# Performance work log

Measured on AMD Instinct MI355X. Metric: run time of the kernel, lower is better.

The kernel has to match this reference:

```python
import jax, jax.numpy as jnp
import numpy as np

N = 64000   # nodes
E = 256000  # edges
G = 2000    # graphs
D = 300     # emb_dim
H = 4       # heads
C = D // H  # head dim = 75
L = 5       # layers
ED = 32     # edge_emb_dim
FD = 256    # feat_dim


def _ln(x, g, b):
    m = x.mean(-1, keepdims=True)
    v = jnp.mean((x - m) ** 2, axis=-1, keepdims=True)
    return (x - m) * jax.lax.rsqrt(v + 1e-5) * g + b


def setup_inputs() -> dict:
    key = jax.random.key(0)
    ks = iter(jax.random.split(key, 48))
    def nrm(shape, s=0.02):
        return jax.random.normal(next(ks), shape, jnp.float32) * s
    inp = {}
    inp["x"] = jax.random.randint(next(ks), (N, 2), 0, 3)
    inp["edge_index"] = jax.random.randint(next(ks), (2, E), 0, N)
    inp["edge_attr"] = jax.random.randint(next(ks), (E, 2), 0, 3)
    inp["batch"] = jnp.sort(jax.random.randint(next(ks), (N,), 0, G))
    inp.update(dict(
        x_emb1=nrm((119, D)), x_emb2=nrm((3, D)),
        e_emb_t=nrm((5, ED)), e_emb_d=nrm((3, ED)),
        edge_proj_w=nrm((ED, ED)), edge_proj_b=nrm((ED,)),
        q_w=nrm((L, D, D)), q_b=nrm((L, D)),
        k_w=nrm((L, D, D)), k_b=nrm((L, D)),
        v_w=nrm((L, D, D)), v_b=nrm((L, D)),
        e_w=nrm((L, ED, D)),
        skip_w=nrm((L, D, D)), skip_b=nrm((L, D)),
        ln1_g=jnp.ones((L, D), jnp.float32), ln1_b=jnp.zeros((L, D), jnp.float32),
        ln2_g=jnp.ones((L, D), jnp.float32), ln2_b=jnp.zeros((L, D), jnp.float32),
        ffn_w1=nrm((L, D, 4 * D)), ffn_b1=nrm((L, 4 * D)),
        ffn_w2=nrm((L, 4 * D, D)), ffn_b2=nrm((L, D)),
        feat_w=nrm((D, FD)), feat_b=nrm((FD,)),
        out_w1=nrm((FD, FD)), out_b1=nrm((FD,)),
        out_w2=nrm((FD, FD // 2)), out_b2=nrm((FD // 2,)),
    ))
    return inp


def reference(x, edge_index, edge_attr, batch, x_emb1, x_emb2, e_emb_t, e_emb_d,
              edge_proj_w, edge_proj_b, q_w, q_b, k_w, k_b, v_w, v_b, e_w,
              skip_w, skip_b, ln1_g, ln1_b, ln2_g, ln2_b,
              ffn_w1, ffn_b1, ffn_w2, ffn_b2, feat_w, feat_b,
              out_w1, out_b1, out_w2, out_b2):
    # node / edge embeddings
    h = x_emb1[x[:, 0]] + x_emb2[x[:, 1]]                               # [N, D]
    ef = (e_emb_t[edge_attr[:, 0]] + e_emb_d[edge_attr[:, 1]]) @ edge_proj_w + edge_proj_b  # [E, ED]
    src, dst = edge_index[0], edge_index[1]
    scale = 1.0 / np.sqrt(C).astype(np.float32)
    for l in range(L):  # loop over fixed layer count
        q = (h @ q_w[l] + q_b[l]).reshape(N, H, C)
        k = (h @ k_w[l] + k_b[l]).reshape(N, H, C)
        v = (h @ v_w[l] + v_b[l]).reshape(N, H, C)
        e = (ef @ e_w[l]).reshape(E, H, C)
        kj = k[src] + e                                                 # [E, H, C]
        alpha = jnp.einsum('ehc,ehc->eh', q[dst], kj) * scale           # [E, H]
        amax = jax.lax.stop_gradient(jax.ops.segment_max(alpha, dst, num_segments=N))
        ea = jnp.exp(alpha - amax[dst])
        den = jax.ops.segment_sum(ea, dst, num_segments=N)
        attn = ea / den[dst]                                            # segment softmax over in-edges of dst
        msg = attn[:, :, None] * (v[src] + e)
        agg = jax.ops.segment_sum(msg, dst, num_segments=N).reshape(N, D)
        conv = agg + h @ skip_w[l] + skip_b[l]                          # TransformerConv with root skip
        h = _ln(h + conv, ln1_g[l], ln1_b[l])
        f = jax.nn.relu(h @ ffn_w1[l] + ffn_b1[l]) @ ffn_w2[l] + ffn_b2[l]
        h = _ln(h + f, ln2_g[l], ln2_b[l])
    cnt = jax.ops.segment_sum(jnp.ones((N,), jnp.float32), batch, num_segments=G)
    g = jax.ops.segment_sum(h, batch, num_segments=G) / jnp.clip(cnt, 1.0)[:, None]
    g = g @ feat_w + feat_b                                             # [G, FD]
    out = jax.nn.relu(g @ out_w1 + out_b1) @ out_w2 + out_b2            # [G, FD//2]
    return (g, out)
```

## Files before the change

### kernel.cpp

```cpp
#include <hip/hip_runtime.h>
#include <hip/hip_bf16.h>
#include <math.h>

typedef __hip_bfloat16 bf16;
typedef unsigned short ushort_t;
typedef unsigned int uint_t;

using bf16x8 = __attribute__((ext_vector_type(8))) __bf16;
using f32x4  = __attribute__((ext_vector_type(4))) float;

constexpr int kN  = 64000;
constexpr int kE  = 256000;
constexpr int kG  = 2000;
constexpr int kD  = 300;
constexpr int kH  = 4;
constexpr int kC  = 75;
constexpr int kL  = 5;
constexpr int kED = 32;
constexpr int kFD = 256;
constexpr int kT  = 15;
constexpr int kDp = 320;
constexpr int kKp2 = 1216;
constexpr int kQV = 1280;
constexpr int kQVn = 1264;
constexpr int kOffK = 300, kOffV = 600, kOffS = 900, kOffQE = 1200;
constexpr int kNpW1 = 1280, kNpW2 = 384;
constexpr int kFDp = 304;

static inline int cdiv(int a, int b) { return (a + b - 1) / b; }

__device__ __forceinline__ ushort_t f2bf(float f) {
    uint_t u = __float_as_uint(f);
    uint_t r = u + 0x7FFFu + ((u >> 16) & 1u);
    return (ushort_t)(r >> 16);
}
__device__ __forceinline__ float bu2f(ushort_t u) {
    return __uint_as_float(((uint_t)u) << 16);
}

__device__ __forceinline__ void gld_lds16(const ushort_t* g, ushort_t* l)
{
    __builtin_amdgcn_global_load_lds(
        (const __attribute__((address_space(1))) void*)g,
        (__attribute__((address_space(3))) void*)(uint_t)(unsigned long long)l,
        16, 0, 0);
}

__global__ void detect_kernel(const uint_t* __restrict__ w, int* __restrict__ flag)
{
    if (threadIdx.x == 0 && blockIdx.x == 0)
        *flag = (w[0] == 0x3F803F80u) ? 1 : 0;
}

__global__ void cvt_kernel(const void* __restrict__ in, float* __restrict__ out,
                           long long n, const int* __restrict__ flag)
{
    long long i = (long long)blockIdx.x * 256 + threadIdx.x;
    if (i >= n) return;
    if (*flag) out[i] = bu2f(((const ushort_t*)in)[i]);
    else       out[i] = ((const float*)in)[i];
}

__global__ void out_write_kernel(const float* __restrict__ in, void* __restrict__ out,
                                 long long n, long long eoff, const int* __restrict__ flag)
{
    long long i = (long long)blockIdx.x * 256 + threadIdx.x;
    if (i >= n) return;
    if (*flag) ((bf16*)out)[eoff + i] = __float2bfloat16(in[i]);
    else       ((float*)out)[eoff + i] = in[i];
}

__global__ void wt_kernel(const void* __restrict__ W, long long elemOff,
                          ushort_t* __restrict__ WT,
                          int K, int N, int ldk, const int* __restrict__ flag)
{
    int i = blockIdx.x * 256 + threadIdx.x;
    if (i >= K * N) return;
    int k = i / N, n = i % N;
    ushort_t val;
    if (*flag) val = ((const ushort_t*)W)[elemOff + i];
    else       val = f2bf(((const float*)W)[elemOff + i]);
    WT[(size_t)n * ldk + k] = val;
}

__global__ void biasqkvs_kernel(const float* __restrict__ qb, const float* __restrict__ kb,
                                const float* __restrict__ vb, const float* __restrict__ sb,
                                float* __restrict__ out)
{
    int i = blockIdx.x * 256 + threadIdx.x;
    if (i >= kL * kQV) return;
    int l = i / kQV, c = i % kQV;
    float v = 0.f;
    if (c < kOffK)          v = qb[l * kD + c];
    else if (c < kOffV)     v = kb[l * kD + c - kOffK];
    else if (c < kOffS)     v = vb[l * kD + c - kOffV];
    else if (c < kOffQE)    v = sb[l * kD + c - kOffS];
    out[i] = v;
}

constexpr int gBM = 128, gBN = 128, gBK = 32;
constexpr int kEpiLd = 136;

__global__ __launch_bounds__(256) void mgemm_kernel(
    const ushort_t* __restrict__ A, int lda,
    const ushort_t* __restrict__ BT, int ldb,
    const float* __restrict__ bias,
    ushort_t* __restrict__ outB, int ldob,
    int M, int N, int K, int relu)
{
    __shared__ ushort_t smem[gBM * kEpiLd];
    ushort_t* As = smem;
    ushort_t* Bs = smem + 8192;

    const int tid  = threadIdx.x;

    const int nxg = gridDim.x;
    int bid;
    {
        int nb = nxg * gridDim.y;
        int orig = blockIdx.y * nxg + blockIdx.x;
        int q8 = nb >> 3, r8 = nb & 7;
        int xcd = orig & 7, lid = orig >> 3;
        bid = (xcd < r8 ? xcd * (q8 + 1) : r8 * (q8 + 1) + (xcd - r8) * q8) + lid;
    }
    const int bm = (bid / nxg) * gBM;
    const int bn = (bid % nxg) * gBN;

    const int wave = tid >> 6, lane = tid & 63;
    const int wr = wave >> 1, wc = wave & 1;
    const int lq = lane & 15, qd = lane >> 4;
    const int qs = (qd ^ ((lq >> 1) & 3)) * 8;

    f32x4 acc[4][4];
#pragma unroll
    for (int i = 0; i < 4; i++)
#pragma unroll
        for (int j = 0; j < 4; j++) acc[i][j] = (f32x4){0.f, 0.f, 0.f, 0.f};

    {
#pragma unroll
        for (int p = 0; p < 2; p++) {
            int u = tid + p * 256;
            gld_lds16(A + (size_t)(bm + (u >> 2)) * lda + ((u ^ (u >> 3)) & 3) * 8, As + u * 8);
        }
#pragma unroll
        for (int p = 0; p < 2; p++) {
            int u = tid + p * 256;
            gld_lds16(BT + (size_t)(bn + (u >> 2)) * ldb + ((u ^ (u >> 3)) & 3) * 8, Bs + u * 8);
        }
    }
    __syncthreads();

    const int nk = K / gBK;
    for (int kt = 0; kt < nk; kt++) {
        const int cb = (kt & 1) * 4096;

        bf16x8 af[4], bfg[4];
#pragma unroll
        for (int i = 0; i < 4; i++)
            af[i] = *reinterpret_cast<const bf16x8*>(&As[cb + (wr * 64 + i * 16 + lq) * gBK + qs]);
#pragma unroll
        for (int j = 0; j < 4; j++)
            bfg[j] = *reinterpret_cast<const bf16x8*>(&Bs[cb + (wc * 64 + j * 16 + lq) * gBK + qs]);

        if (kt + 1 < nk) {
            const int k0 = (kt + 1) * gBK;
            const int nb2 = cb ^ 4096;
#pragma unroll
            for (int p = 0; p < 2; p++) {
                int u = tid + p * 256;
                gld_lds16(A + (size_t)(bm + (u >> 2)) * lda + k0 + ((u ^ (u >> 3)) & 3) * 8,
                          As + nb2 + u * 8);
            }
#pragma unroll
            for (int p = 0; p < 2; p++) {
                int u = tid + p * 256;
                gld_lds16(BT + (size_t)(bn + (u >> 2)) * ldb + k0 + ((u ^ (u >> 3)) & 3) * 8,
                          Bs + nb2 + u * 8);
            }
        }

#pragma unroll
        for (int i = 0; i < 4; i++)
#pragma unroll
            for (int j = 0; j < 4; j++)
                acc[i][j] = __builtin_amdgcn_mfma_f32_16x16x32_bf16(af[i], bfg[j], acc[i][j], 0, 0, 0);

        __syncthreads();
    }

#pragma unroll
    for (int i = 0; i < 4; i++) {
#pragma unroll
        for (int j = 0; j < 4; j++) {
            int lcol = wc * 64 + j * 16 + lq;
            int gcol = bn + lcol;
            float bv = (bias && gcol < N) ? bias[gcol] : 0.f;
#pragma unroll
            for (int r2 = 0; r2 < 4; r2++) {
                int lrow = wr * 64 + i * 16 + qd * 4 + r2;
                float v = acc[i][j][r2] + bv;
                if (relu) v = fmaxf(v, 0.f);
                smem[lrow * kEpiLd + lcol] = f2bf(v);
            }
        }
    }
    __syncthreads();
#pragma unroll
    for (int s = 0; s < 8; s++) {
        int seg  = tid + s * 256;
        int lrow = seg >> 4;
        int loff = (seg & 15) * 8;
        int gcol = bn + loff;
        if (gcol + 8 <= ldob) {
            bf16x8 pv = *reinterpret_cast<const bf16x8*>(&smem[lrow * kEpiLd + loff]);
            *reinterpret_cast<bf16x8*>(&outB[(size_t)(bm + lrow) * ldob + gcol]) = pv;
        }
    }
}

__global__ __launch_bounds__(256) void gemm_kernel(
    const float* __restrict__ A, const float* __restrict__ W,
    const float* __restrict__ bias, float* __restrict__ C,
    int M, int N, int K, int relu)
{
    constexpr int BM = 64, BN = 64, BK = 16;
    __shared__ float As[BK][BM + 1];
    __shared__ float Bs[BK][BN + 1];
    const int bm = blockIdx.y * BM;
    const int bn = blockIdx.x * BN;
    const int tid = threadIdx.x;
    const int tr = tid / 16;
    const int tc = tid % 16;
    float acc[4][4] = {};
    for (int k0 = 0; k0 < K; k0 += BK) {
        for (int t = tid; t < BM * BK; t += 256) {
            int r = t / BK, c = t % BK;
            int gr = bm + r, gc = k0 + c;
            As[c][r] = (gr < M && gc < K) ? A[(size_t)gr * K + gc] : 0.f;
        }
        for (int t = tid; t < BK * BN; t += 256) {
            int r = t / BN, c = t % BN;
            int gr = k0 + r, gc = bn + c;
            Bs[r][c] = (gr < K && gc < N) ? W[(size_t)gr * N + gc] : 0.f;
        }
        __syncthreads();
#pragma unroll
        for (int k = 0; k < BK; k++) {
            float a[4], b[4];
#pragma unroll
            for (int i = 0; i < 4; i++) a[i] = As[k][tr * 4 + i];
#pragma unroll
            for (int j = 0; j < 4; j++) b[j] = Bs[k][tc * 4 + j];
#pragma unroll
            for (int i = 0; i < 4; i++)
#pragma unroll
                for (int j = 0; j < 4; j++) acc[i][j] += a[i] * b[j];
        }
        __syncthreads();
    }
#pragma unroll
    for (int i = 0; i < 4; i++) {
        int gr = bm + tr * 4 + i;
        if (gr >= M) continue;
#pragma unroll
        for (int j = 0; j < 4; j++) {
            int gc = bn + tc * 4 + j;
            if (gc >= N) continue;
            float v = acc[i][j];
            if (bias) v += bias[gc];
            if (relu) v = fmaxf(v, 0.f);
            C[(size_t)gr * N + gc] = v;
        }
    }
}

__global__ void node_embed_kernel(const int* __restrict__ x,
                                  const float* __restrict__ emb1,
                                  const float* __restrict__ emb2,
                                  ushort_t* __restrict__ hb)
{
    long long i = (long long)blockIdx.x * blockDim.x + threadIdx.x;
    if (i >= (long long)kN * kD) return;
    int n = (int)(i / kD), d = (int)(i % kD);
    float v = emb1[(size_t)x[n * 2] * kD + d] + emb2[(size_t)x[n * 2 + 1] * kD + d];
    hb[(size_t)n * kDp + d] = f2bf(v);
}

__global__ void eftab_kernel(const float* __restrict__ emb_t, const float* __restrict__ emb_d,
                             const float* __restrict__ pw, const float* __restrict__ pb,
                             float* __restrict__ eftab)
{
    int tid = threadIdx.x;
    if (tid >= kT * kED) return;
    int t = tid / kED, j = tid % kED;
    int a0 = t / 3, a1 = t % 3;
    float acc = pb[j];
#pragma unroll
    for (int k = 0; k < kED; k++) {
        float s = emb_t[a0 * kED + k] + emb_d[a1 * kED + k];
        acc += s * pw[k * kED + j];
    }
    eftab[tid] = acc;
}

__global__ __launch_bounds__(256) void etab_kernel(const float* __restrict__ eftab,
                                                   const float* __restrict__ ew,
                                                   float* __restrict__ etab)
{
    __shared__ float se[kT * kED];
    for (int i = threadIdx.x; i < kT * kED; i += 256) se[i] = eftab[i];
    __syncthreads();
    for (int o = threadIdx.x; o < kT * kD; o += 256) {
        int t = o / kD, d = o % kD;
        float acc = 0.f;
#pragma unroll
        for (int k = 0; k < kED; k++) acc += se[t * kED + k] * ew[k * kD + d];
        etab[o] = acc;
    }
}

__global__ void etabT2_kernel(const float* __restrict__ etab, ushort_t* __restrict__ out)
{
    int i = blockIdx.x * 256 + threadIdx.x;
    if (i >= 64 * kDp) return;
    int j = i / kDp, k = i % kDp;
    ushort_t v = 0;
    if (j < kT * kH && k < kD) {
        int t = j >> 2, hh = j & 3;
        if (k >= hh * kC && k < hh * kC + kC) v = f2bf(etab[t * kD + k]);
    }
    out[i] = v;
}

__global__ void izero_kernel(int* __restrict__ p, int n)
{
    int i = blockIdx.x * 256 + threadIdx.x;
    if (i < n) p[i] = 0;
}

__global__ void deg_kernel(const int* __restrict__ dst, int* __restrict__ deg)
{
    int e = blockIdx.x * 256 + threadIdx.x;
    if (e >= kE) return;
    atomicAdd(&deg[dst[e]], 1);
}

__global__ __launch_bounds__(256) void scan1_kernel(const int* __restrict__ deg, int* __restrict__ bsum)
{
    __shared__ int s[256];
    int i = blockIdx.x * 256 + threadIdx.x;
    s[threadIdx.x] = (i < kN) ? deg[i] : 0;
    __syncthreads();
    for (int off = 128; off > 0; off >>= 1) {
        if (threadIdx.x < off) s[threadIdx.x] += s[threadIdx.x + off];
        __syncthreads();
    }
    if (threadIdx.x == 0) bsum[blockIdx.x] = s[0];
}

__global__ __launch_bounds__(256) void scan2_kernel(const int* __restrict__ bsum, int* __restrict__ boff,
                                                    int nb, int* __restrict__ row_ptr)
{
    __shared__ int s[256];
    int tid = threadIdx.x;
    int v = (tid < nb) ? bsum[tid] : 0;
    s[tid] = v;
    __syncthreads();
    for (int off = 1; off < 256; off <<= 1) {
        int t = (tid >= off) ? s[tid - off] : 0;
        __syncthreads();
        s[tid] += t;
        __syncthreads();
    }
    if (tid < nb) boff[tid] = s[tid] - v;
    if (tid == 255) row_ptr[kN] = s[255];
}

__global__ __launch_bounds__(256) void scan3_kernel(const int* __restrict__ deg, const int* __restrict__ boff,
                                                    int* __restrict__ row_ptr)
{
    __shared__ int s[256];
    int tid = threadIdx.x;
    int i = blockIdx.x * 256 + tid;
    int v = (i < kN) ? deg[i] : 0;
    s[tid] = v;
    __syncthreads();
    for (int off = 1; off < 256; off <<= 1) {
        int t = (tid >= off) ? s[tid - off] : 0;
        __syncthreads();
        s[tid] += t;
        __syncthreads();
    }
    if (i < kN) row_ptr[i] = boff[blockIdx.x] + s[tid] - v;
}

__global__ void poscopy_kernel(const int* __restrict__ row_ptr, int* __restrict__ pos)
{
    int i = blockIdx.x * 256 + threadIdx.x;
    if (i < kN) pos[i] = row_ptr[i];
}

__global__ void fill_kernel(const int* __restrict__ src, const int* __restrict__ dst,
                            const int* __restrict__ edge_attr,
                            int* __restrict__ pos, int* __restrict__ cpack)
{
    int e = blockIdx.x * 256 + threadIdx.x;
    if (e >= kE) return;
    int d = dst[e];
    int slot = atomicAdd(&pos[d], 1);
    cpack[slot] = (src[e] << 8) | (edge_attr[e * 2] * 3 + edge_attr[e * 2 + 1]);
}

__global__ void gptr_kernel(const int* __restrict__ batch, int* __restrict__ gptr)
{
    int i = blockIdx.x * 256 + threadIdx.x;
    if (i >= kN) return;
    int b1 = batch[i];
    int b0 = (i == 0) ? -1 : batch[i - 1];
    for (int g = b0 + 1; g <= b1; g++) gptr[g] = i;
    if (i == kN - 1)
        for (int g = b1 + 1; g <= kG; g++) gptr[g] = kN;
}

__global__ __launch_bounds__(256) void gsln_kernel(
    const int* __restrict__ row_ptr, const int* __restrict__ cpack,
    const ushort_t* __restrict__ qkvs,
    const float* __restrict__ etab,
    const float* __restrict__ g, const float* __restrict__ b,
    ushort_t* __restrict__ hb)
{
    __shared__ float sE[kT * kD];
    for (int i = threadIdx.x; i < kT * kD; i += 256) sE[i] = etab[i];
    __syncthreads();
    const int wslot = threadIdx.x >> 6, lane = threadIdx.x & 63;
    const int hh = lane >> 4, sub = lane & 15;
    const float scale = 0.11547005383792516f;

    int idxj[5];
    bool vj[5];
#pragma unroll
    for (int j = 0; j < 5; j++) {
        int o = sub + 16 * j;
        vj[j] = (o < kC);
        idxj[j] = hh * kC + (vj[j] ? o : 0);
    }

    for (int it = 0; it < 4; it++) {
        int n = blockIdx.x * 4 + wslot + it * 16000;
        int beg = row_ptr[n], end = row_ptr[n + 1];
        const ushort_t* qrow = qkvs + (size_t)n * kQV;

        float qv[5];
#pragma unroll
        for (int j = 0; j < 5; j++)
            qv[j] = vj[j] ? bu2f(qrow[idxj[j]]) : 0.f;

        float acc[5] = {0.f, 0.f, 0.f, 0.f, 0.f};
        float den = 0.f;
        for (int i = beg; i < end; i++) {
            int pk = cpack[i];
            int s = pk >> 8, t = pk & 255;
            const ushort_t* srow = qkvs + (size_t)s * kQV;
            float hp = 0.f;
#pragma unroll
            for (int j = 0; j < 5; j++)
                if (vj[j]) hp += qv[j] * bu2f(srow[kOffK + idxj[j]]);
            hp += __shfl_xor(hp, 1, 64);
            hp += __shfl_xor(hp, 2, 64);
            hp += __shfl_xor(hp, 4, 64);
            hp += __shfl_xor(hp, 8, 64);
            float a = (hp + bu2f(qrow[kOffQE + t * kH + hh])) * scale;
            a = fminf(fmaxf(a, -60.f), 60.f);
            float eh = expf(a);
            den += eh;
            const float* ep = sE + t * kD;
#pragma unroll
            for (int j = 0; j < 5; j++)
                if (vj[j]) acc[j] += eh * (bu2f(srow[kOffV + idxj[j]]) + ep[idxj[j]]);
        }

        const float inv_den = (den > 0.f) ? 1.f / den : 0.f;
        const ushort_t* skipp = qrow + kOffS;
        float vals[5], sum = 0.f;
#pragma unroll
        for (int j = 0; j < 5; j++) {
            float tV = 0.f;
            if (vj[j])
                tV = bu2f(hb[(size_t)n * kDp + idxj[j]]) + acc[j] * inv_den + bu2f(skipp[idxj[j]]);
            vals[j] = tV;
            sum += tV;
        }
        for (int off = 1; off < 64; off <<= 1) sum += __shfl_xor(sum, off, 64);
        float mean = sum / kD;
        float var = 0.f;
#pragma unroll
        for (int j = 0; j < 5; j++) {
            if (vj[j]) { float dv = vals[j] - mean; var += dv * dv; }
        }
        for (int off = 1; off < 64; off <<= 1) var += __shfl_xor(var, off, 64);
        float rstd = rsqrtf(var / kD + 1e-5f);
#pragma unroll
        for (int j = 0; j < 5; j++) {
            if (vj[j])
                hb[(size_t)n * kDp + idxj[j]] =
                    f2bf((vals[j] - mean) * rstd * g[idxj[j]] + b[idxj[j]]);
        }
    }
}

__global__ __launch_bounds__(256) void ln2_kernel(
    ushort_t* hb, const ushort_t* __restrict__ f, int ldf,
    const float* __restrict__ g, const float* __restrict__ b)
{
    int row  = (blockIdx.x * blockDim.x + threadIdx.x) >> 6;
    int lane = threadIdx.x & 63;
    if (row >= kN) return;
    size_t baseH = (size_t)row * kDp;
    size_t baseF = (size_t)row * ldf;
    float vals[5];
    float sum = 0.f;
#pragma unroll
    for (int i = 0; i < 5; i++) {
        int idx = lane + i * 64;
        float t = 0.f;
        if (idx < kD) t = bu2f(hb[baseH + idx]) + bu2f(f[baseF + idx]);
        vals[i] = t;
        sum += t;
    }
    for (int off = 1; off < 64; off <<= 1) sum += __shfl_xor(sum, off, 64);
    float mean = sum / kD;
    float var = 0.f;
#pragma unroll
    for (int i = 0; i < 5; i++) {
        int idx = lane + i * 64;
        if (idx < kD) { float dv = vals[i] - mean; var += dv * dv; }
    }
    for (int off = 1; off < 64; off <<= 1) var += __shfl_xor(var, off, 64);
    float rstd = rsqrtf(var / kD + 1e-5f);
#pragma unroll
    for (int i = 0; i < 5; i++) {
        int idx = lane + i * 64;
        if (idx < kD)
            hb[baseH + idx] = f2bf((vals[i] - mean) * rstd * g[idx] + b[idx]);
    }
}

__global__ void zero_kernel(float* __restrict__ p, long long n)
{
    long long i = (long long)blockIdx.x * blockDim.x + threadIdx.x;
    if (i < n) p[i] = 0.f;
}

__global__ __launch_bounds__(256) void pool2_kernel(const ushort_t* __restrict__ hb,
                                                    const int* __restrict__ gptr,
                                                    float* __restrict__ pooled)
{
    int g = blockIdx.x;
    int beg = gptr[g], end = gptr[g + 1];
    float inv = (end > beg) ? 1.f / (float)(end - beg) : 0.f;
    for (int d = threadIdx.x; d < kD; d += 256) {
        float acc = 0.f;
        for (int n = beg; n < end; n++)
            acc += bu2f(hb[(size_t)n * kDp + d]);
        pooled[(size_t)g * kD + d] = acc * inv;
    }
}

extern "C" void kernel_launch(void* const* d_in, const int* in_sizes, int n_in,
                              void* d_out, int out_size, void* d_ws, size_t ws_size,
                              hipStream_t stream)
{
    const int* x          = (const int*)d_in[0];
    const int* edge_index = (const int*)d_in[1];
    const int* edge_attr  = (const int*)d_in[2];
    const int* batch      = (const int*)d_in[3];
    const int* src = edge_index;
    const int* dst = edge_index + kE;

    float* ws = (float*)d_ws;
    size_t off = 0;
    int* flag = (int*)(ws + off); off += 16;
    const bool big[33] = {false,false,false,false,false,false,false,false,false,false,
                          true, false, true, false, true, false, false, true, false, false,
                          false,false,false, true, false, true, false,false,false,false,
                          false,false,false};
    float* canon[33] = {};
    for (int i = 4; i < 33; i++) {
        if (big[i]) continue;
        canon[i] = ws + off; off += (size_t)in_sizes[i];
    }
    off = (off + 3) & ~(size_t)3;
    int* deg     = (int*)(ws + off); off += (size_t)kN;
    int* row_ptr = (int*)(ws + off); off += (size_t)kN + 4;
    int* pos     = (int*)(ws + off); off += (size_t)kN;
    int* cpack   = (int*)(ws + off); off += (size_t)kE;
    int* bsum    = (int*)(ws + off); off += 256;
    int* boff    = (int*)(ws + off); off += 256;
    int* gptr    = (int*)(ws + off); off += (size_t)kG + 4;
    float* eftab = ws + off; off += (size_t)kT * kED;
    float* etab5 = ws + off; off += (size_t)kL * kT * kD;
    float* bqv5  = ws + off; off += (size_t)kL * kQV;
    off = (off + 3) & ~(size_t)3;
    ushort_t* hb   = (ushort_t*)(ws + off); off += (size_t)kN * kDp / 2;
    ushort_t* QV   = (ushort_t*)(ws + off); off += (size_t)kN * kQV / 2;
    ushort_t* fbuf = (ushort_t*)(ws + off); off += (size_t)kN * kFDp / 2;
    ushort_t* warena = (ushort_t*)(ws + off);
    ushort_t* wqv5 = warena;
    ushort_t* wt15 = wqv5 + (size_t)kL * kQV * kDp;
    ushort_t* wt25 = wt15 + (size_t)kL * kNpW1 * kDp;
    size_t warena_ushorts = (size_t)kL * (kQV + kNpW1) * kDp + (size_t)kL * kNpW2 * kKp2;
    off += warena_ushorts / 2 + 4;
    float* pooled = (float*)QV;
    float* gbuf   = pooled + (size_t)kG * kD;
    float* t1     = gbuf + (size_t)kG * kFD;
    float* o2     = t1 + (size_t)kG * kFD;

    detect_kernel<<<1, 64, 0, stream>>>((const uint_t*)d_in[19], flag);
    for (int i = 4; i < 33; i++) {
        if (big[i]) continue;
        long long n = in_sizes[i];
        cvt_kernel<<<cdiv((int)n, 256), 256, 0, stream>>>(d_in[i], canon[i], n, flag);
    }

    const long long ND = (long long)kN * kD;

    auto mgemm = [&](const ushort_t* A, int lda, const ushort_t* BT, int ldb,
                     const float* bias, ushort_t* outB, int ldob,
                     int M, int N, int K, int relu) {
        dim3 grid(cdiv(N, 128), M / 128);
        mgemm_kernel<<<grid, 256, 0, stream>>>(A, lda, BT, ldb, bias, outB, ldob, M, N, K, relu);
    };
    auto gemm = [&](const float* A, const float* W, const float* bias, float* C,
                    int M, int N, int K, int relu) {
        dim3 grid(cdiv(N, 64), cdiv(M, 64));
        gemm_kernel<<<grid, 256, 0, stream>>>(A, W, bias, C, M, N, K, relu);
    };

    node_embed_kernel<<<cdiv((int)ND, 256), 256, 0, stream>>>(x, canon[4], canon[5], hb);
    eftab_kernel<<<1, 512, 0, stream>>>(canon[6], canon[7], canon[8], canon[9], eftab);

    const int nb = cdiv(kN, 256);
    izero_kernel<<<cdiv(kN, 256), 256, 0, stream>>>(deg, kN);
    deg_kernel<<<cdiv(kE, 256), 256, 0, stream>>>(dst, deg);
    scan1_kernel<<<nb, 256, 0, stream>>>(deg, bsum);
    scan2_kernel<<<1, 256, 0, stream>>>(bsum, boff, nb, row_ptr);
    scan3_kernel<<<nb, 256, 0, stream>>>(deg, boff, row_ptr);
    poscopy_kernel<<<cdiv(kN, 256), 256, 0, stream>>>(row_ptr, pos);
    fill_kernel<<<cdiv(kE, 256), 256, 0, stream>>>(src, dst, edge_attr, pos, cpack);
    gptr_kernel<<<cdiv(kN, 256), 256, 0, stream>>>(batch, gptr);

    zero_kernel<<<cdiv((int)(warena_ushorts / 2), 256) + 1, 256, 0, stream>>>(
        (float*)warena, (long long)(warena_ushorts / 2));
    for (int l = 0; l < kL; l++) {
        ushort_t* wqv = wqv5 + (size_t)l * kQV * kDp;
        ushort_t* w1  = wt15 + (size_t)l * kNpW1 * kDp;
        ushort_t* w2  = wt25 + (size_t)l * kNpW2 * kKp2;
        float* etab   = etab5 + (size_t)l * kT * kD;
        wt_kernel<<<cdiv(kD * kD, 256), 256, 0, stream>>>(d_in[10], (long long)l * kD * kD, wqv, kD, kD, kDp, flag);
        wt_kernel<<<cdiv(kD * kD, 256), 256, 0, stream>>>(d_in[12], (long long)l * kD * kD, wqv + (size_t)kOffK * kDp, kD, kD, kDp, flag);
        wt_kernel<<<cdiv(kD * kD, 256), 256, 0, stream>>>(d_in[14], (long long)l * kD * kD, wqv + (size_t)kOffV * kDp, kD, kD, kDp, flag);
        wt_kernel<<<cdiv(kD * kD, 256), 256, 0, stream>>>(d_in[17], (long long)l * kD * kD, wqv + (size_t)kOffS * kDp, kD, kD, kDp, flag);
        wt_kernel<<<cdiv(kD * 1200, 256), 256, 0, stream>>>(d_in[23], (long long)l * kD * 1200, w1, kD, 1200, kDp, flag);
        wt_kernel<<<cdiv(1200 * kD, 256), 256, 0, stream>>>(d_in[25], (long long)l * 1200 * kD, w2, 1200, kD, kKp2, flag);
        etab_kernel<<<1, 256, 0, stream>>>(eftab, canon[16] + (size_t)l * kED * kD, etab);
        etabT2_kernel<<<cdiv(64 * kDp, 256), 256, 0, stream>>>(etab, wqv + (size_t)kOffQE * kDp);
    }
    biasqkvs_kernel<<<cdiv(kL * kQV, 256), 256, 0, stream>>>(
        canon[11], canon[13], canon[15], canon[18], bqv5);

    for (int l = 0; l < kL; l++) {
        const ushort_t* wqv = wqv5 + (size_t)l * kQV * kDp;
        const ushort_t* w1  = wt15 + (size_t)l * kNpW1 * kDp;
        const ushort_t* w2  = wt25 + (size_t)l * kNpW2 * kKp2;
        const float* etab = etab5 + (size_t)l * kT * kD;

        mgemm(hb, kDp, wqv, kDp, bqv5 + (size_t)l * kQV, QV, kQV, kN, kQVn, kDp, 0);

        gsln_kernel<<<4000, 256, 0, stream>>>(row_ptr, cpack, QV, etab,
            canon[19] + (size_t)l * kD, canon[20] + (size_t)l * kD, hb);

        ushort_t* mid = QV;
        mgemm(hb, kDp, w1, kDp, canon[24] + (size_t)l * 1200, mid, kKp2,
              kN, 1200, kDp, 1);
        mgemm(mid, kKp2, w2, kKp2, canon[26] + (size_t)l * kD, fbuf, kFDp,
              kN, kD, kKp2, 0);

        ln2_kernel<<<kN / 4, 256, 0, stream>>>(hb, fbuf, kFDp,
            canon[21] + (size_t)l * kD, canon[22] + (size_t)l * kD);
    }

    pool2_kernel<<<kG, 256, 0, stream>>>(hb, gptr, pooled);

    gemm(pooled, canon[27], canon[28], gbuf, kG, kFD, kD, 0);
    gemm(gbuf, canon[29], canon[30], t1, kG, kFD, kFD, 1);
    gemm(t1, canon[31], canon[32], o2, kG, kFD / 2, kFD, 0);

    out_write_kernel<<<cdiv(kG * kFD, 256), 256, 0, stream>>>(
        gbuf, d_out, (long long)kG * kFD, 0, flag);
    out_write_kernel<<<cdiv(kG * kFD / 2, 256), 256, 0, stream>>>(
        o2, d_out, (long long)kG * (kFD / 2), (long long)kG * kFD, flag);
}
```

Measured before the change: 2.564 ms.

## Fuse FFN up and down projections into one kernel keeping intermediate in LDS

Replaces the two FFN GEMMs with a single fused kernel. Each 1024-thread block handles 128 rows. It computes relu(h@W1+b1) in 128-column chunks, stages each chunk in shared memory as bf16, and accumulates it straight into the W2 projection. This removes the write and re-read of the N x 1216 intermediate through global memory. In exchange, A and W operands are read directly from global memory without LDS tiling, and only 500 blocks launch, which may limit occupancy and MFMA efficiency.

```diff
diff --git a/kernel.cpp b/kernel.cpp
--- a/kernel.cpp
+++ b/kernel.cpp
@@ -20,11 +20,11 @@
 constexpr int kFD = 256;
 constexpr int kT  = 15;
 constexpr int kDp = 320;
-constexpr int kKp2 = 1216;
 constexpr int kQV = 1280;
 constexpr int kQVn = 1264;
 constexpr int kOffK = 300, kOffV = 600, kOffS = 900, kOffQE = 1200;
 constexpr int kNpW1 = 1280, kNpW2 = 384;
+constexpr int kW2ld = 1280;
 constexpr int kFDp = 304;
 
 static inline int cdiv(int a, int b) { return (a + b - 1) / b; }
@@ -216,6 +216,131 @@
             bf16x8 pv = *reinterpret_cast<const bf16x8*>(&smem[lrow * kEpiLd + loff]);
             *reinterpret_cast<bf16x8*>(&outB[(size_t)(bm + lrow) * ldob + gcol]) = pv;
         }
+    }
+}
+
+__global__ __launch_bounds__(1024) void ffn_kernel(
+    const ushort_t* __restrict__ A,
+    const ushort_t* __restrict__ W1T,
+    const ushort_t* __restrict__ W2T,
+    const float* __restrict__ b1,
+    const float* __restrict__ b2,
+    ushort_t* __restrict__ outF)
+{
+    __shared__ ushort_t sm[64 * 328];
+
+    int bid;
+    {
+        int nb = gridDim.x, orig = blockIdx.x;
+        int q8 = nb >> 3, r8 = nb & 7;
+        int xcd = orig & 7, lid = orig >> 3;
+        bid = (xcd < r8 ? xcd * (q8 + 1) : r8 * (q8 + 1) + (xcd - r8) * q8) + lid;
+    }
+    const int bm = bid * 128;
+
+    const int tid  = threadIdx.x;
+    const int wave = tid >> 6, lane = tid & 63;
+    const int wr = wave >> 2, wc = wave & 3;
+    const int lq = lane & 15, qd = lane >> 4, qk = qd * 8;
+
+    f32x4 acc2[2][5];
+#pragma unroll
+    for (int i = 0; i < 2; i++)
+#pragma unroll
+        for (int j = 0; j < 5; j++) acc2[i][j] = (f32x4){0.f, 0.f, 0.f, 0.f};
+
+    const ushort_t* a0 = A + (size_t)(bm + wr * 32 + lq) * kDp;
+    const ushort_t* a1 = A + (size_t)(bm + wr * 32 + 16 + lq) * kDp;
+
+    for (int j = 0; j < 10; j++) {
+        const int jc = j * 128;
+
+        f32x4 macc[2][2];
+#pragma unroll
+        for (int i = 0; i < 2; i++)
+#pragma unroll
+            for (int q = 0; q < 2; q++) macc[i][q] = (f32x4){0.f, 0.f, 0.f, 0.f};
+
+        const ushort_t* w1p0 = W1T + (size_t)(jc + wc * 32 + lq) * kDp;
+        const ushort_t* w1p1 = w1p0 + (size_t)16 * kDp;
+#pragma unroll 2
+        for (int kt = 0; kt < 10; kt++) {
+            const int ko = kt * 32 + qk;
+            bf16x8 af0 = *reinterpret_cast<const bf16x8*>(a0 + ko);
+            bf16x8 af1 = *reinterpret_cast<const bf16x8*>(a1 + ko);
+            bf16x8 bg0 = *reinterpret_cast<const bf16x8*>(w1p0 + ko);
+            bf16x8 bg1 = *reinterpret_cast<const bf16x8*>(w1p1 + ko);
+            macc[0][0] = __builtin_amdgcn_mfma_f32_16x16x32_bf16(af0, bg0, macc[0][0], 0, 0, 0);
+            macc[0][1] = __builtin_amdgcn_mfma_f32_16x16x32_bf16(af0, bg1, macc[0][1], 0, 0, 0);
+            macc[1][0] = __builtin_amdgcn_mfma_f32_16x16x32_bf16(af1, bg0, macc[1][0], 0, 0, 0);
+            macc[1][1] = __builtin_amdgcn_mfma_f32_16x16x32_bf16(af1, bg1, macc[1][1], 0, 0, 0);
+        }
+
+        float bv1[2];
+#pragma unroll
+        for (int q = 0; q < 2; q++) {
+            int c1 = jc + wc * 32 + q * 16 + lq;
+            bv1[q] = (c1 < 1200) ? b1[c1] : 0.f;
+        }
+#pragma unroll
+        for (int i = 0; i < 2; i++)
+#pragma unroll
+            for (int q = 0; q < 2; q++)
+#pragma unroll
+                for (int r2 = 0; r2 < 4; r2++) {
+                    int row = wr * 32 + i * 16 + qd * 4 + r2;
+                    int col = wc * 32 + q * 16 + lq;
+                    sm[row * 136 + col] = f2bf(fmaxf(macc[i][q][r2] + bv1[q], 0.f));
+                }
+        __syncthreads();
+
+#pragma unroll 2
+        for (int kt2 = 0; kt2 < 4; kt2++) {
+            const int ko = kt2 * 32 + qk;
+            bf16x8 mf0 = *reinterpret_cast<const bf16x8*>(&sm[(wr * 32 + lq) * 136 + ko]);
+            bf16x8 mf1 = *reinterpret_cast<const bf16x8*>(&sm[(wr * 32 + 16 + lq) * 136 + ko]);
+#pragma unroll
+            for (int j5 = 0; j5 < 5; j5++) {
+                bf16x8 wg = *reinterpret_cast<const bf16x8*>(
+                    W2T + (size_t)(wc * 80 + j5 * 16 + lq) * kW2ld + jc + ko);
+                acc2[0][j5] = __builtin_amdgcn_mfma_f32_16x16x32_bf16(mf0, wg, acc2[0][j5], 0, 0, 0);
+                acc2[1][j5] = __builtin_amdgcn_mfma_f32_16x16x32_bf16(mf1, wg, acc2[1][j5], 0, 0, 0);
+            }
+        }
+        __syncthreads();
+    }
+
+    float bv2[5];
+#pragma unroll
+    for (int j5 = 0; j5 < 5; j5++) {
+        int col = wc * 80 + j5 * 16 + lq;
+        bv2[j5] = (col < kD) ? b2[col] : 0.f;
+    }
+#pragma unroll
+    for (int h = 0; h < 2; h++) {
+        if ((wr >> 1) == h) {
+#pragma unroll
+            for (int i = 0; i < 2; i++)
+#pragma unroll
+                for (int j5 = 0; j5 < 5; j5++)
+#pragma unroll
+                    for (int r2 = 0; r2 < 4; r2++) {
+                        int row = (wr & 1) * 32 + i * 16 + qd * 4 + r2;
+                        int col = wc * 80 + j5 * 16 + lq;
+                        sm[row * 328 + col] = f2bf(acc2[i][j5][r2] + bv2[j5]);
+                    }
+        }
+        __syncthreads();
+#pragma unroll
+        for (int p = 0; p < 3; p++) {
+            int seg = tid + p * 1024;
+            if (seg < 64 * 38) {
+                int row = seg / 38, c8 = (seg % 38) * 8;
+                bf16x8 pv = *reinterpret_cast<const bf16x8*>(&sm[row * 328 + c8]);
+                *reinterpret_cast<bf16x8*>(&outF[(size_t)(bm + h * 64 + row) * kFDp + c8]) = pv;
+            }
+        }
+        __syncthreads();
     }
 }
 
@@ -609,7 +734,7 @@
     ushort_t* wqv5 = warena;
     ushort_t* wt15 = wqv5 + (size_t)kL * kQV * kDp;
     ushort_t* wt25 = wt15 + (size_t)kL * kNpW1 * kDp;
-    size_t warena_ushorts = (size_t)kL * (kQV + kNpW1) * kDp + (size_t)kL * kNpW2 * kKp2;
+    size_t warena_ushorts = (size_t)kL * (kQV + kNpW1) * kDp + (size_t)kL * kNpW2 * kW2ld;
     off += warena_ushorts / 2 + 4;
     float* pooled = (float*)QV;
     float* gbuf   = pooled + (size_t)kG * kD;
@@ -655,14 +780,14 @@
     for (int l = 0; l < kL; l++) {
         ushort_t* wqv = wqv5 + (size_t)l * kQV * kDp;
         ushort_t* w1  = wt15 + (size_t)l * kNpW1 * kDp;
-        ushort_t* w2  = wt25 + (size_t)l * kNpW2 * kKp2;
+        ushort_t* w2  = wt25 + (size_t)l * kNpW2 * kW2ld;
         float* etab   = etab5 + (size_t)l * kT * kD;
         wt_kernel<<<cdiv(kD * kD, 256), 256, 0, stream>>>(d_in[10], (long long)l * kD * kD, wqv, kD, kD, kDp, flag);
         wt_kernel<<<cdiv(kD * kD, 256), 256, 0, stream>>>(d_in[12], (long long)l * kD * kD, wqv + (size_t)kOffK * kDp, kD, kD, kDp, flag);
         wt_kernel<<<cdiv(kD * kD, 256), 256, 0, stream>>>(d_in[14], (long long)l * kD * kD, wqv + (size_t)kOffV * kDp, kD, kD, kDp, flag);
         wt_kernel<<<cdiv(kD * kD, 256), 256, 0, stream>>>(d_in[17], (long long)l * kD * kD, wqv + (size_t)kOffS * kDp, kD, kD, kDp, flag);
         wt_kernel<<<cdiv(kD * 1200, 256), 256, 0, stream>>>(d_in[23], (long long)l * kD * 1200, w1, kD, 1200, kDp, flag);
-        wt_kernel<<<cdiv(1200 * kD, 256), 256, 0, stream>>>(d_in[25], (long long)l * 1200 * kD, w2, 1200, kD, kKp2, flag);
+        wt_kernel<<<cdiv(1200 * kD, 256), 256, 0, stream>>>(d_in[25], (long long)l * 1200 * kD, w2, 1200, kD, kW2ld, flag);
         etab_kernel<<<1, 256, 0, stream>>>(eftab, canon[16] + (size_t)l * kED * kD, etab);
         etabT2_kernel<<<cdiv(64 * kDp, 256), 256, 0, stream>>>(etab, wqv + (size_t)kOffQE * kDp);
     }
@@ -672,7 +797,7 @@
     for (int l = 0; l < kL; l++) {
         const ushort_t* wqv = wqv5 + (size_t)l * kQV * kDp;
         const ushort_t* w1  = wt15 + (size_t)l * kNpW1 * kDp;
-        const ushort_t* w2  = wt25 + (size_t)l * kNpW2 * kKp2;
+        const ushort_t* w2  = wt25 + (size_t)l * kNpW2 * kW2ld;
         const float* etab = etab5 + (size_t)l * kT * kD;
 
         mgemm(hb, kDp, wqv, kDp, bqv5 + (size_t)l * kQV, QV, kQV, kN, kQVn, kDp, 0);
@@ -680,11 +805,8 @@
         gsln_kernel<<<4000, 256, 0, stream>>>(row_ptr, cpack, QV, etab,
             canon[19] + (size_t)l * kD, canon[20] + (size_t)l * kD, hb);
 
-        ushort_t* mid = QV;
-        mgemm(hb, kDp, w1, kDp, canon[24] + (size_t)l * 1200, mid, kKp2,
-              kN, 1200, kDp, 1);
-        mgemm(mid, kKp2, w2, kKp2, canon[26] + (size_t)l * kD, fbuf, kFDp,
-              kN, kD, kKp2, 0);
+        ffn_kernel<<<500, 1024, 0, stream>>>(hb, w1, w2,
+            canon[24] + (size_t)l * 1200, canon[26] + (size_t)l * kD, fbuf);
 
         ln2_kernel<<<kN / 4, 256, 0, stream>>>(hb, fbuf, kFDp,
             canon[21] + (size_t)l * kD, canon[22] + (size_t)l * kD);
```

After: 4.474 ms. +74.5%, slower.

## Fuse FFN second GEMM with residual LayerNorm and batch edge gather loop

Applied to the files above, without the earlier changes.

Replaces the separate FFN down-projection GEMM plus ln2 kernel with one kernel. It computes a 128-row by 320-column tile with MFMA, then applies bias, the residual add and LayerNorm from shared memory, so the fbuf intermediate no longer makes a round trip through global memory. Separately, the attention gather loop now processes four edges per iteration with batched loads, interleaved shuffles and a fast exp, to expose more memory-level parallelism. The fused kernel uses large shared memory and 20 accumulators per thread, which may limit occupancy, and it adds a zeroing pass over hb.

```diff
diff --git a/kernel.cpp b/kernel.cpp
--- a/kernel.cpp
+++ b/kernel.cpp
@@ -25,7 +25,7 @@
 constexpr int kQVn = 1264;
 constexpr int kOffK = 300, kOffV = 600, kOffS = 900, kOffQE = 1200;
 constexpr int kNpW1 = 1280, kNpW2 = 384;
-constexpr int kFDp = 304;
+constexpr int kW2ld = 1280;
 
 static inline int cdiv(int a, int b) { return (a + b - 1) / b; }
 
@@ -216,6 +216,131 @@
             bf16x8 pv = *reinterpret_cast<const bf16x8*>(&smem[lrow * kEpiLd + loff]);
             *reinterpret_cast<bf16x8*>(&outB[(size_t)(bm + lrow) * ldob + gcol]) = pv;
         }
+    }
+}
+
+__global__ __launch_bounds__(512, 4) void ffn2ln_kernel(
+    const ushort_t* __restrict__ A,
+    const ushort_t* __restrict__ BT,
+    const float* __restrict__ b2,
+    ushort_t* hb,
+    const float* __restrict__ g, const float* __restrict__ b)
+{
+    __shared__ ushort_t smem[28672];
+    ushort_t* As = smem;
+    ushort_t* Bs = smem + 8192;
+
+    int bid;
+    {
+        int nb = gridDim.x, orig = blockIdx.x;
+        int q8 = nb >> 3, r8 = nb & 7;
+        int xcd = orig & 7, lid = orig >> 3;
+        bid = (xcd < r8 ? xcd * (q8 + 1) : r8 * (q8 + 1) + (xcd - r8) * q8) + lid;
+    }
+    const int bm = bid * 128;
+
+    const int tid  = threadIdx.x;
+    const int wave = tid >> 6, lane = tid & 63;
+    const int wr = wave >> 1, wc = wave & 1;
+    const int lq = lane & 15, qd = lane >> 4;
+    const int qs = (qd ^ ((lq >> 1) & 3)) * 8;
+
+    auto stage = [&](int kt, int buf) {
+        const int k0 = kt * 32;
+        {
+            int u = tid;
+            gld_lds16(A + (size_t)(bm + (u >> 2)) * kKp2 + k0 + ((u ^ (u >> 3)) & 3) * 8,
+                      As + buf * 4096 + u * 8);
+        }
+#pragma unroll
+        for (int p = 0; p < 3; p++) {
+            int u = tid + p * 512;
+            if (u < 1280)
+                gld_lds16(BT + (size_t)(u >> 2) * kW2ld + k0 + ((u ^ (u >> 3)) & 3) * 8,
+                          Bs + buf * 10240 + u * 8);
+        }
+    };
+
+    f32x4 acc[2][10];
+#pragma unroll
+    for (int i = 0; i < 2; i++)
+#pragma unroll
+        for (int f = 0; f < 10; f++) acc[i][f] = (f32x4){0.f, 0.f, 0.f, 0.f};
+
+    stage(0, 0);
+    __syncthreads();
+
+    for (int kt = 0; kt < kKp2 / 32; kt++) {
+        const int cur = kt & 1;
+        bf16x8 af0 = *reinterpret_cast<const bf16x8*>(
+            &As[cur * 4096 + (wr * 32 + lq) * 32 + qs]);
+        bf16x8 af1 = *reinterpret_cast<const bf16x8*>(
+            &As[cur * 4096 + (wr * 32 + 16 + lq) * 32 + qs]);
+        if (kt + 1 < kKp2 / 32) stage(kt + 1, cur ^ 1);
+#pragma unroll
+        for (int f = 0; f < 10; f++) {
+            bf16x8 bfg = *reinterpret_cast<const bf16x8*>(
+                &Bs[cur * 10240 + (wc * 160 + f * 16 + lq) * 32 + qs]);
+            acc[0][f] = __builtin_amdgcn_mfma_f32_16x16x32_bf16(af0, bfg, acc[0][f], 0, 0, 0);
+            acc[1][f] = __builtin_amdgcn_mfma_f32_16x16x32_bf16(af1, bfg, acc[1][f], 0, 0, 0);
+        }
+        __syncthreads();
+    }
+
+    float bv[10];
+#pragma unroll
+    for (int f = 0; f < 10; f++) {
+        int col = wc * 160 + f * 16 + lq;
+        bv[f] = (col < kD) ? b2[col] : 0.f;
+    }
+    const int team = tid >> 6;
+#pragma unroll
+    for (int h = 0; h < 2; h++) {
+        if ((wr >> 1) == h) {
+#pragma unroll
+            for (int i = 0; i < 2; i++)
+#pragma unroll
+                for (int f = 0; f < 10; f++)
+#pragma unroll
+                    for (int r2 = 0; r2 < 4; r2++) {
+                        int row = (wr & 1) * 32 + i * 16 + qd * 4 + r2;
+                        int col = wc * 160 + f * 16 + lq;
+                        smem[row * 328 + col] = f2bf(acc[i][f][r2] + bv[f]);
+                    }
+        }
+        __syncthreads();
+        for (int r = 0; r < 8; r++) {
+            int rl = team * 8 + r;
+            int n = bm + h * 64 + rl;
+            size_t baseH = (size_t)n * kDp;
+            float vals[5];
+            float sum = 0.f;
+#pragma unroll
+            for (int i5 = 0; i5 < 5; i5++) {
+                int idx = lane + i5 * 64;
+                float t = 0.f;
+                if (idx < kD) t = bu2f(hb[baseH + idx]) + bu2f(smem[rl * 328 + idx]);
+                vals[i5] = t;
+                sum += t;
+            }
+            for (int off2 = 1; off2 < 64; off2 <<= 1) sum += __shfl_xor(sum, off2, 64);
+            float mean = sum / kD;
+            float var = 0.f;
+#pragma unroll
+            for (int i5 = 0; i5 < 5; i5++) {
+                int idx = lane + i5 * 64;
+                if (idx < kD) { float dv = vals[i5] - mean; var += dv * dv; }
+            }
+            for (int off2 = 1; off2 < 64; off2 <<= 1) var += __shfl_xor(var, off2, 64);
+            float rstd = rsqrtf(var / kD + 1e-5f);
+#pragma unroll
+            for (int i5 = 0; i5 < 5; i5++) {
+                int idx = lane + i5 * 64;
+                if (idx < kD)
+                    hb[baseH + idx] = f2bf((vals[i5] - mean) * rstd * g[idx] + b[idx]);
+            }
+        }
+        __syncthreads();
     }
 }
 
@@ -458,26 +583,58 @@
 
         float acc[5] = {0.f, 0.f, 0.f, 0.f, 0.f};
         float den = 0.f;
-        for (int i = beg; i < end; i++) {
-            int pk = cpack[i];
-            int s = pk >> 8, t = pk & 255;
-            const ushort_t* srow = qkvs + (size_t)s * kQV;
-            float hp = 0.f;
-#pragma unroll
-            for (int j = 0; j < 5; j++)
-                if (vj[j]) hp += qv[j] * bu2f(srow[kOffK + idxj[j]]);
-            hp += __shfl_xor(hp, 1, 64);
-            hp += __shfl_xor(hp, 2, 64);
-            hp += __shfl_xor(hp, 4, 64);
-            hp += __shfl_xor(hp, 8, 64);
-            float a = (hp + bu2f(qrow[kOffQE + t * kH + hh])) * scale;
-            a = fminf(fmaxf(a, -60.f), 60.f);
-            float eh = expf(a);
-            den += eh;
-            const float* ep = sE + t * kD;
-#pragma unroll
-            for (int j = 0; j < 5; j++)
-                if (vj[j]) acc[j] += eh * (bu2f(srow[kOffV + idxj[j]]) + ep[idxj[j]]);
+        for (int i = beg; i < end; i += 4) {
+            int pk[4];
+            float ehm[4];
+#pragma unroll
+            for (int e = 0; e < 4; e++) {
+                bool hv = (i + e < end);
+                pk[e] = cpack[hv ? i + e : i];
+                ehm[e] = hv ? 1.f : 0.f;
+            }
+            const ushort_t* sr[4];
+            int tt[4];
+#pragma unroll
+            for (int e = 0; e < 4; e++) {
+                sr[e] = qkvs + (size_t)(pk[e] >> 8) * kQV;
+                tt[e] = pk[e] & 255;
+            }
+            float kv[4][5];
+#pragma unroll
+            for (int e = 0; e < 4; e++)
+#pragma unroll
+                for (int j = 0; j < 5; j++)
+                    kv[e][j] = vj[j] ? bu2f(sr[e][kOffK + idxj[j]]) : 0.f;
+            float qe[4];
+#pragma unroll
+            for (int e = 0; e < 4; e++)
+                qe[e] = bu2f(qrow[kOffQE + tt[e] * kH + hh]);
+
+            float hp[4] = {0.f, 0.f, 0.f, 0.f};
+#pragma unroll
+            for (int e = 0; e < 4; e++)
+#pragma unroll
+                for (int j = 0; j < 5; j++) hp[e] += qv[j] * kv[e][j];
+#pragma unroll
+            for (int m = 1; m <= 8; m <<= 1) {
+#pragma unroll
+                for (int e = 0; e < 4; e++) hp[e] += __shfl_xor(hp[e], m, 64);
+            }
+            float eh[4];
+#pragma unroll
+            for (int e = 0; e < 4; e++) {
+                float a = fminf(fmaxf((hp[e] + qe[e]) * scale, -60.f), 60.f);
+                eh[e] = __expf(a) * ehm[e];
+                den += eh[e];
+            }
+#pragma unroll
+            for (int e = 0; e < 4; e++) {
+                const float* ep = sE + tt[e] * kD;
+#pragma unroll
+                for (int j = 0; j < 5; j++)
+                    if (vj[j])
+                        acc[j] += eh[e] * (bu2f(sr[e][kOffV + idxj[j]]) + ep[idxj[j]]);
+            }
         }
 
         const float inv_den = (den > 0.f) ? 1.f / den : 0.f;
@@ -506,43 +663,6 @@
                 hb[(size_t)n * kDp + idxj[j]] =
                     f2bf((vals[j] - mean) * rstd * g[idxj[j]] + b[idxj[j]]);
         }
-    }
-}
-
-__global__ __launch_bounds__(256) void ln2_kernel(
-    ushort_t* hb, const ushort_t* __restrict__ f, int ldf,
-    const float* __restrict__ g, const float* __restrict__ b)
-{
-    int row  = (blockIdx.x * blockDim.x + threadIdx.x) >> 6;
-    int lane = threadIdx.x & 63;
-    if (row >= kN) return;
-    size_t baseH = (size_t)row * kDp;
-    size_t baseF = (size_t)row * ldf;
-    float vals[5];
-    float sum = 0.f;
-#pragma unroll
-    for (int i = 0; i < 5; i++) {
-        int idx = lane + i * 64;
-        float t = 0.f;
-        if (idx < kD) t = bu2f(hb[baseH + idx]) + bu2f(f[baseF + idx]);
-        vals[i] = t;
-        sum += t;
-    }
-    for (int off = 1; off < 64; off <<= 1) sum += __shfl_xor(sum, off, 64);
-    float mean = sum / kD;
-    float var = 0.f;
-#pragma unroll
-    for (int i = 0; i < 5; i++) {
-        int idx = lane + i * 64;
-        if (idx < kD) { float dv = vals[i] - mean; var += dv * dv; }
-    }
-    for (int off = 1; off < 64; off <<= 1) var += __shfl_xor(var, off, 64);
-    float rstd = rsqrtf(var / kD + 1e-5f);
-#pragma unroll
-    for (int i = 0; i < 5; i++) {
-        int idx = lane + i * 64;
-        if (idx < kD)
-            hb[baseH + idx] = f2bf((vals[i] - mean) * rstd * g[idx] + b[idx]);
     }
 }
 
@@ -604,12 +724,11 @@
     off = (off + 3) & ~(size_t)3;
     ushort_t* hb   = (ushort_t*)(ws + off); off += (size_t)kN * kDp / 2;
     ushort_t* QV   = (ushort_t*)(ws + off); off += (size_t)kN * kQV / 2;
-    ushort_t* fbuf = (ushort_t*)(ws + off); off += (size_t)kN * kFDp / 2;
     ushort_t* warena = (ushort_t*)(ws + off);
     ushort_t* wqv5 = warena;
     ushort_t* wt15 = wqv5 + (size_t)kL * kQV * kDp;
     ushort_t* wt25 = wt15 + (size_t)kL * kNpW1 * kDp;
-    size_t warena_ushorts = (size_t)kL * (kQV + kNpW1) * kDp + (size_t)kL * kNpW2 * kKp2;
+    size_t warena_ushorts = (size_t)kL * (kQV + kNpW1) * kDp + (size_t)kL * kNpW2 * kW2ld;
     off += warena_ushorts / 2 + 4;
     float* pooled = (float*)QV;
     float* gbuf   = pooled + (size_t)kG * kD;
@@ -637,6 +756,8 @@
         gemm_kernel<<<grid, 256, 0, stream>>>(A, W, bias, C, M, N, K, relu);
     };
 
+    zero_kernel<<<cdiv((int)((long long)kN * kDp / 2), 256), 256, 0, stream>>>(
+        (float*)hb, (long long)kN * kDp / 2);
     node_embed_kernel<<<cdiv((int)ND, 256), 256, 0, stream>>>(x, canon[4], canon[5], hb);
     eftab_kernel<<<1, 512, 0, stream>>>(canon[6], canon[7], canon[8], canon[9], eftab);
 
@@ -655,14 +776,14 @@
     for (int l = 0; l < kL; l++) {
         ushort_t* wqv = wqv5 + (size_t)l * kQV * kDp;
         ushort_t* w1  = wt15 + (size_t)l * kNpW1 * kDp;
-        ushort_t* w2  = wt25 + (size_t)l * kNpW2 * kKp2;
+        ushort_t* w2  = wt25 + (size_t)l * kNpW2 * kW2ld;
         float* etab   = etab5 + (size_t)l * kT * kD;
         wt_kernel<<<cdiv(kD * kD, 256), 256, 0, stream>>>(d_in[10], (long long)l * kD * kD, wqv, kD, kD, kDp, flag);
         wt_kernel<<<cdiv(kD * kD, 256), 256, 0, stream>>>(d_in[12], (long long)l * kD * kD, wqv + (size_t)kOffK * kDp, kD, kD, kDp, flag);
         wt_kernel<<<cdiv(kD * kD, 256), 256, 0, stream>>>(d_in[14], (long long)l * kD * kD, wqv + (size_t)kOffV * kDp, kD, kD, kDp, flag);
         wt_kernel<<<cdiv(kD * kD, 256), 256, 0, stream>>>(d_in[17], (long long)l * kD * kD, wqv + (size_t)kOffS * kDp, kD, kD, kDp, flag);
         wt_kernel<<<cdiv(kD * 1200, 256), 256, 0, stream>>>(d_in[23], (long long)l * kD * 1200, w1, kD, 1200, kDp, flag);
-        wt_kernel<<<cdiv(1200 * kD, 256), 256, 0, stream>>>(d_in[25], (long long)l * 1200 * kD, w2, 1200, kD, kKp2, flag);
+        wt_kernel<<<cdiv(1200 * kD, 256), 256, 0, stream>>>(d_in[25], (long long)l * 1200 * kD, w2, 1200, kD, kW2ld, flag);
         etab_kernel<<<1, 256, 0, stream>>>(eftab, canon[16] + (size_t)l * kED * kD, etab);
         etabT2_kernel<<<cdiv(64 * kDp, 256), 256, 0, stream>>>(etab, wqv + (size_t)kOffQE * kDp);
     }
@@ -672,7 +793,7 @@
     for (int l = 0; l < kL; l++) {
         const ushort_t* wqv = wqv5 + (size_t)l * kQV * kDp;
         const ushort_t* w1  = wt15 + (size_t)l * kNpW1 * kDp;
-        const ushort_t* w2  = wt25 + (size_t)l * kNpW2 * kKp2;
+        const ushort_t* w2  = wt25 + (size_t)l * kNpW2 * kW2ld;
         const float* etab = etab5 + (size_t)l * kT * kD;
 
         mgemm(hb, kDp, wqv, kDp, bqv5 + (size_t)l * kQV, QV, kQV, kN, kQVn, kDp, 0);
@@ -683,10 +804,9 @@
         ushort_t* mid = QV;
         mgemm(hb, kDp, w1, kDp, canon[24] + (size_t)l * 1200, mid, kKp2,
               kN, 1200, kDp, 1);
-        mgemm(mid, kKp2, w2, kKp2, canon[26] + (size_t)l * kD, fbuf, kFDp,
-              kN, kD, kKp2, 0);
-
-        ln2_kernel<<<kN / 4, 256, 0, stream>>>(hb, fbuf, kFDp,
+
+        ffn2ln_kernel<<<kN / 128, 512, 0, stream>>>(mid, w2,
+            canon[26] + (size_t)l * kD, hb,
             canon[21] + (size_t)l * kD, canon[22] + (size_t)l * kD);
     }
 
```

After: 2.644 ms. 1.03x slower.
